# Kernel optimization log

Measured on AMD Instinct MI355X. Metric: run time of the kernel, lower is better.

## Reference

```python
import jax, jax.numpy as jnp
import numpy as np

N = 8192
IN_F = 512
OUT_F = 128
NEG_BIG = -9.0e15


def setup_inputs() -> dict:
    key = jax.random.key(0)
    k_x, k_adj, k_w, k_a1, k_a2 = jax.random.split(key, 5)
    X = jax.random.normal(k_x, (N, IN_F), dtype=jnp.float32)
    adj = jax.random.randint(k_adj, (N, N), 0, 2, dtype=jnp.int32)
    # xavier_uniform with gain=1.414
    gain = 1.414
    lim_w = gain * np.sqrt(6.0 / (IN_F + OUT_F))
    W = jax.random.uniform(k_w, (IN_F, OUT_F), minval=-lim_w, maxval=lim_w, dtype=jnp.float32)
    lim_a = gain * np.sqrt(6.0 / (OUT_F + 1))
    a_1 = jax.random.uniform(k_a1, (OUT_F, 1), minval=-lim_a, maxval=lim_a, dtype=jnp.float32)
    a_2 = jax.random.uniform(k_a2, (OUT_F, 1), minval=-lim_a, maxval=lim_a, dtype=jnp.float32)
    return {"X": X, "adj": adj, "W": W, "a_1": a_1, "a_2": a_2}


def reference(X, adj, W, a_1, a_2):
    h = X @ W                         # [N, out]
    Wh1 = h @ a_1                     # [N, 1]
    Wh2 = h @ a_2                     # [N, 1]
    alpha = Wh1 + Wh2.T               # [N, N] broadcast score sum
    s = jax.nn.sigmoid(alpha)
    masked = jnp.where(adj > 0, s, jnp.float32(NEG_BIG))
    attn = jax.nn.softmax(masked, axis=1)  # dropout p=0.0 -> identity
    return attn @ h                   # [N, out]
```

## Files before the change

### kernel.cpp

```cpp
#include <hip/hip_runtime.h>
#include <hip/hip_bf16.h>

#define N_NODES 8192
#define IN_F 512
#define OUT_F 128
#define KP 16
#define KT_PER 16
#define NWORDS (N_NODES / 32)
#define LOG2E 1.4426950408889634f

typedef unsigned short u16;
typedef unsigned int u32;
typedef short s16x8 __attribute__((ext_vector_type(8)));
typedef float f32x4 __attribute__((ext_vector_type(4)));
typedef u32 u32x4 __attribute__((ext_vector_type(4)));

__device__ __forceinline__ u16 f2bf(float f) {
    union { float f; unsigned u; } x; x.f = f;
    unsigned r = x.u + 0x7FFFu + ((x.u >> 16) & 1u);
    return (u16)(r >> 16);
}

__device__ __forceinline__ u32 packbf2(float a, float b) {
    __hip_bfloat162 h = __float22bfloat162_rn(make_float2(a, b));
    u32 u; __builtin_memcpy(&u, &h, 4);
    return u;
}

__device__ __forceinline__ float edge_p(float wh1, float w2, int keep) {
    float alpha = wh1 + w2;
    float e = exp2f(-LOG2E * alpha);
    float s = __builtin_amdgcn_rcpf(1.0f + e);
    float p = exp2f(LOG2E * s);
    return keep ? p : 0.0f;
}

__global__ __launch_bounds__(256)
void prep(const int* __restrict__ adj, const float* __restrict__ W,
          const float* __restrict__ a1, const float* __restrict__ a2,
          u32* __restrict__ Pk, u16* __restrict__ W_frag,
          float* __restrict__ Wa1, float* __restrict__ Wa2) {
    int b = blockIdx.x;
    int tid = threadIdx.x;
    if (b < 8192) {
        int gid = b * 256 + tid;
        const int* src = adj + (size_t)gid * 32;
        u32 bits = 0;
        #pragma unroll
        for (int t = 0; t < 8; t++) {
            int4 v = *(const int4*)(src + t * 4);
            bits |= (u32)(v.x > 0) << (t * 4 + 0);
            bits |= (u32)(v.y > 0) << (t * 4 + 1);
            bits |= (u32)(v.z > 0) << (t * 4 + 2);
            bits |= (u32)(v.w > 0) << (t * 4 + 3);
        }
        Pk[gid] = bits;
    } else if (b < 8448) {
        int t2 = (b - 8192) * 256 + tid;
        int j = t2 & 7;
        int lane = (t2 >> 3) & 63;
        int nt = (t2 >> 9) & 7;
        int kt = t2 >> 12;
        int k = kt * 32 + (lane >> 4) * 8 + j;
        int n = nt * 16 + (lane & 15);
        W_frag[t2] = f2bf(W[k * OUT_F + n]);
    } else {
        int k = (b - 8448) * 256 + tid;
        float s1 = 0.f, s2 = 0.f;
        #pragma unroll 8
        for (int n = 0; n < OUT_F; n++) {
            float w = W[k * OUT_F + n];
            s1 += w * a1[n];
            s2 += w * a2[n];
        }
        Wa1[k] = s1; Wa2[k] = s2;
    }
}

__global__ __launch_bounds__(512)
void gemm_h(const float* __restrict__ X, const u16* __restrict__ W_frag,
            const float* __restrict__ Wa1, const float* __restrict__ Wa2,
            float* __restrict__ Wh1, float* __restrict__ Wh2,
            u16* __restrict__ h_frag) {
    int tid = threadIdx.x;
    int wave = tid >> 6;
    int lane = tid & 63;
    int quad = lane >> 4;
    int lid = lane & 15;
    int rbase = blockIdx.x * 16;
    const float* xrow = X + (size_t)(rbase + lid) * IN_F;
    const s16x8* Wf = (const s16x8*)W_frag;
    f32x4 acc = {};
    float p1 = 0.f, p2 = 0.f;
    int nt0 = wave;

    int k0p = quad * 8;
    float4 X0 = *(const float4*)(xrow + k0p);
    float4 X1 = *(const float4*)(xrow + k0p + 4);
    s16x8 B0 = Wf[nt0 * 64 + lane];
    float4 A0 = {}, A1 = {}, C0 = {}, C1 = {};
    if (wave == 0) {
        A0 = *(const float4*)(Wa1 + k0p); A1 = *(const float4*)(Wa1 + k0p + 4);
        C0 = *(const float4*)(Wa2 + k0p); C1 = *(const float4*)(Wa2 + k0p + 4);
    }

    #pragma unroll 1
    for (int kt = 0; kt < 16; kt++) {
        float4 x0 = X0, x1 = X1;
        s16x8 b0 = B0;
        float4 wa = A0, wb = A1, wc = C0, wd = C1;
        int ktn = (kt + 1 < 16) ? kt + 1 : kt;
        int k0n = ktn * 32 + quad * 8;
        X0 = *(const float4*)(xrow + k0n);
        X1 = *(const float4*)(xrow + k0n + 4);
        B0 = Wf[(ktn * 8 + nt0) * 64 + lane];
        if (wave == 0) {
            A0 = *(const float4*)(Wa1 + k0n); A1 = *(const float4*)(Wa1 + k0n + 4);
            C0 = *(const float4*)(Wa2 + k0n); C1 = *(const float4*)(Wa2 + k0n + 4);
        }

        u32x4 uv;
        uv.x = packbf2(x0.x, x0.y); uv.y = packbf2(x0.z, x0.w);
        uv.z = packbf2(x1.x, x1.y); uv.w = packbf2(x1.z, x1.w);
        s16x8 a = __builtin_bit_cast(s16x8, uv);
        if (wave == 0) {
            p1 += x0.x*wa.x + x0.y*wa.y + x0.z*wa.z + x0.w*wa.w
                + x1.x*wb.x + x1.y*wb.y + x1.z*wb.z + x1.w*wb.w;
            p2 += x0.x*wc.x + x0.y*wc.y + x0.z*wc.z + x0.w*wc.w
                + x1.x*wd.x + x1.y*wd.y + x1.z*wd.z + x1.w*wd.w;
        }
        acc = __builtin_amdgcn_mfma_f32_16x16x32_bf16(a, b0, acc, 0, 0, 0);
    }

    #pragma unroll
    for (int reg = 0; reg < 4; reg++) {
        int row = rbase + quad * 4 + reg;
        int ktile = row >> 5, kl = row & 31;
        int lane2 = (kl >> 3) * 16 + lid, j2 = kl & 7;
        h_frag[(size_t)((ktile * 8 + nt0) * 64 + lane2) * 8 + j2] = f2bf(acc[reg]);
    }
    if (wave == 0) {
        p1 += __shfl_xor(p1, 16, 64); p1 += __shfl_xor(p1, 32, 64);
        p2 += __shfl_xor(p2, 16, 64); p2 += __shfl_xor(p2, 32, 64);
        if (lane < 16) { Wh1[rbase + lid] = p1; Wh2[rbase + lid] = p2; }
    }
}

__global__ __launch_bounds__(256)
void attn_kernel(const u32* __restrict__ Pk, const float* __restrict__ Wh1,
                 const float* __restrict__ Wh2, const u16* __restrict__ h_frag,
                 float* __restrict__ out_part, float* __restrict__ sum_part) {
    int tid = threadIdx.x;
    int wave = tid >> 6;
    int lane = tid & 63;
    int quad = lane >> 4;
    int lid = lane & 15;
    int rtile = blockIdx.x >> 4;
    int kh = blockIdx.x & (KP - 1);
    int rbase = rtile * 128 + wave * 32;
    int r0 = rbase + lid, r1 = r0 + 16;

    float wh10 = Wh1[r0], wh11 = Wh1[r1];
    f32x4 acc0[8] = {}, acc1[8] = {};
    float ps0 = 0.f, ps1 = 0.f;
    const s16x8* Hf = (const s16x8*)h_frag;
    const u32* prow0 = Pk + (size_t)r0 * NWORDS;
    const u32* prow1 = Pk + (size_t)r1 * NWORDS;
    const int kt0 = kh * KT_PER;

    u32x4 PA = *(const u32x4*)(prow0 + kt0);
    u32x4 PB = *(const u32x4*)(prow1 + kt0);

    auto step = [&](int i, u32 pw0, u32 pw1) {
        int kt = kt0 + i;
        int k0 = kt * 32 + quad * 8;
        float4 w20 = *(const float4*)(Wh2 + k0);
        float4 w21 = *(const float4*)(Wh2 + k0 + 4);
        u32 w0 = pw0 >> (quad * 8);
        u32 w1 = pw1 >> (quad * 8);

        float e0 = edge_p(wh10, w20.x, (w0 >> 0) & 1);
        float e1 = edge_p(wh10, w20.y, (w0 >> 1) & 1);
        float e2 = edge_p(wh10, w20.z, (w0 >> 2) & 1);
        float e3 = edge_p(wh10, w20.w, (w0 >> 3) & 1);
        float e4 = edge_p(wh10, w21.x, (w0 >> 4) & 1);
        float e5 = edge_p(wh10, w21.y, (w0 >> 5) & 1);
        float e6 = edge_p(wh10, w21.z, (w0 >> 6) & 1);
        float e7 = edge_p(wh10, w21.w, (w0 >> 7) & 1);
        ps0 += ((e0 + e1) + (e2 + e3)) + ((e4 + e5) + (e6 + e7));
        u32x4 uv0;
        uv0.x = packbf2(e0, e1); uv0.y = packbf2(e2, e3);
        uv0.z = packbf2(e4, e5); uv0.w = packbf2(e6, e7);

        float f0 = edge_p(wh11, w20.x, (w1 >> 0) & 1);
        float f1 = edge_p(wh11, w20.y, (w1 >> 1) & 1);
        float f2 = edge_p(wh11, w20.z, (w1 >> 2) & 1);
        float f3 = edge_p(wh11, w20.w, (w1 >> 3) & 1);
        float f4 = edge_p(wh11, w21.x, (w1 >> 4) & 1);
        float f5 = edge_p(wh11, w21.y, (w1 >> 5) & 1);
        float f6 = edge_p(wh11, w21.z, (w1 >> 6) & 1);
        float f7 = edge_p(wh11, w21.w, (w1 >> 7) & 1);
        ps1 += ((f0 + f1) + (f2 + f3)) + ((f4 + f5) + (f6 + f7));
        u32x4 uv1;
        uv1.x = packbf2(f0, f1); uv1.y = packbf2(f2, f3);
        uv1.z = packbf2(f4, f5); uv1.w = packbf2(f6, f7);

        s16x8 af0 = __builtin_bit_cast(s16x8, uv0);
        s16x8 af1 = __builtin_bit_cast(s16x8, uv1);

        #pragma unroll
        for (int nt = 0; nt < 8; nt++) {
            s16x8 b = Hf[(kt * 8 + nt) * 64 + lane];
            acc0[nt] = __builtin_amdgcn_mfma_f32_16x16x32_bf16(af0, b, acc0[nt], 0, 0, 0);
            acc1[nt] = __builtin_amdgcn_mfma_f32_16x16x32_bf16(af1, b, acc1[nt], 0, 0, 0);
        }
    };

    #pragma unroll 1
    for (int g = 0; g < KT_PER / 4; g++) {
        u32x4 cPA = PA, cPB = PB;
        int gb = kt0 + ((g + 1 < KT_PER / 4) ? (g + 1) * 4 : 0);
        PA = *(const u32x4*)(prow0 + gb);
        PB = *(const u32x4*)(prow1 + gb);
        step(g * 4 + 0, cPA.x, cPB.x);
        step(g * 4 + 1, cPA.y, cPB.y);
        step(g * 4 + 2, cPA.z, cPB.z);
        step(g * 4 + 3, cPA.w, cPB.w);
    }

    ps0 += __shfl_xor(ps0, 16, 64); ps0 += __shfl_xor(ps0, 32, 64);
    ps1 += __shfl_xor(ps1, 16, 64); ps1 += __shfl_xor(ps1, 32, 64);
    if (quad == 0) {
        sum_part[(size_t)kh * N_NODES + r0] = ps0;
        sum_part[(size_t)kh * N_NODES + r1] = ps1;
    }

    #pragma unroll
    for (int nt = 0; nt < 8; nt++) {
        #pragma unroll
        for (int reg = 0; reg < 4; reg++) {
            int row0 = rbase + quad * 4 + reg;
            int col = nt * 16 + lid;
            out_part[((size_t)kh * N_NODES + row0) * OUT_F + col] = acc0[nt][reg];
            out_part[((size_t)kh * N_NODES + row0 + 16) * OUT_F + col] = acc1[nt][reg];
        }
    }
}

__global__ void finalize(const float* __restrict__ out_part,
                         const float* __restrict__ sum_part,
                         float* __restrict__ out) {
    int gid = blockIdx.x * 256 + threadIdx.x;
    int i = gid >> 7;
    float s = 0.f, v = 0.f;
    for (int kh = 0; kh < KP; kh++) {
        s += sum_part[(size_t)kh * N_NODES + i];
        v += out_part[(size_t)kh * N_NODES * OUT_F + gid];
    }
    out[gid] = v / s;
}

extern "C" void kernel_launch(void* const* d_in, const int* in_sizes, int n_in,
                              void* d_out, int out_size, void* d_ws, size_t ws_size,
                              hipStream_t stream) {
    const float* X   = (const float*)d_in[0];
    const int*   adj = (const int*)d_in[1];
    const float* W   = (const float*)d_in[2];
    const float* a1  = (const float*)d_in[3];
    const float* a2  = (const float*)d_in[4];

    char* ws = (char*)d_ws;
    float* Wh1 = (float*)(ws);
    float* Wh2 = (float*)(ws + (32 << 10));
    float* Wa1 = (float*)(ws + (64 << 10));
    float* Wa2 = (float*)(ws + (66 << 10));
    u16* W_frag = (u16*)(ws + (128 << 10));
    u16* h_frag = (u16*)(ws + (256 << 10));
    u32* Pk     = (u32*)(ws + ((size_t)4 << 20));
    float* out_part = (float*)(ws + ((size_t)16 << 20));
    float* sum_part = (float*)(ws + ((size_t)80 << 20));
    float* out = (float*)d_out;

    hipLaunchKernelGGL(prep, dim3(8450), dim3(256), 0, stream,
                       adj, W, a1, a2, Pk, W_frag, Wa1, Wa2);
    hipLaunchKernelGGL(gemm_h, dim3(512), dim3(512), 0, stream,
                       X, W_frag, Wa1, Wa2, Wh1, Wh2, h_frag);
    hipLaunchKernelGGL(attn_kernel, dim3(64 * KP), dim3(256), 0, stream,
                       Pk, Wh1, Wh2, h_frag, out_part, sum_part);
    hipLaunchKernelGGL(finalize, dim3((N_NODES * OUT_F) / 256), dim3(256), 0, stream,
                       out_part, sum_part, out);
}
```

Baseline: 461.9 us.

## Stage h fragments in LDS, halve K-split, restructure gemm_h with LDS X tiles

The attention kernel now splits K into 8 parts instead of 16. It double-buffers h_frag tiles and Wh2 slices in shared memory, staged cooperatively by all four waves, so they are no longer each loaded per wave from global memory. gemm_h keeps W fragments in registers, stages bf16-packed X tiles through double-buffered LDS, and does 32 rows per block. The Wh1/Wh2 dot products move to separate extra blocks. This cuts redundant global traffic and partial-sum volume, at the cost of less grid parallelism in attention, more LDS and register pressure, and explicit barriers.

```diff
diff --git a/kernel.cpp b/kernel.cpp
--- a/kernel.cpp
+++ b/kernel.cpp
@@ -4,8 +4,8 @@
 #define N_NODES 8192
 #define IN_F 512
 #define OUT_F 128
-#define KP 16
-#define KT_PER 16
+#define KP 8
+#define KT_PER 32
 #define NWORDS (N_NODES / 32)
 #define LOG2E 1.4426950408889634f
 
@@ -77,59 +77,69 @@
     }
 }
 
-__global__ __launch_bounds__(512)
+__global__ __launch_bounds__(512, 2)
 void gemm_h(const float* __restrict__ X, const u16* __restrict__ W_frag,
             const float* __restrict__ Wa1, const float* __restrict__ Wa2,
             float* __restrict__ Wh1, float* __restrict__ Wh2,
             u16* __restrict__ h_frag) {
     int tid = threadIdx.x;
+    if (blockIdx.x >= 256) {
+        int r = (blockIdx.x - 256) * 512 + tid;
+        const float4* xr = (const float4*)(X + (size_t)r * IN_F);
+        const float4* a4 = (const float4*)Wa1;
+        const float4* b4 = (const float4*)Wa2;
+        float s1 = 0.f, s2 = 0.f;
+        #pragma unroll 4
+        for (int i = 0; i < 128; i++) {
+            float4 x = xr[i], a = a4[i], bb = b4[i];
+            s1 += x.x*a.x + x.y*a.y + x.z*a.z + x.w*a.w;
+            s2 += x.x*bb.x + x.y*bb.y + x.z*bb.z + x.w*bb.w;
+        }
+        Wh1[r] = s1; Wh2[r] = s2;
+        return;
+    }
+
+    __shared__ u32x4 AXL[2][512];
     int wave = tid >> 6;
     int lane = tid & 63;
     int quad = lane >> 4;
     int lid = lane & 15;
-    int rbase = blockIdx.x * 16;
-    const float* xrow = X + (size_t)(rbase + lid) * IN_F;
+    int rbase = blockIdx.x * 32;
     const s16x8* Wf = (const s16x8*)W_frag;
-    f32x4 acc = {};
-    float p1 = 0.f, p2 = 0.f;
-    int nt0 = wave;
-
-    int k0p = quad * 8;
-    float4 X0 = *(const float4*)(xrow + k0p);
-    float4 X1 = *(const float4*)(xrow + k0p + 4);
-    s16x8 B0 = Wf[nt0 * 64 + lane];
-    float4 A0 = {}, A1 = {}, C0 = {}, C1 = {};
-    if (wave == 0) {
-        A0 = *(const float4*)(Wa1 + k0p); A1 = *(const float4*)(Wa1 + k0p + 4);
-        C0 = *(const float4*)(Wa2 + k0p); C1 = *(const float4*)(Wa2 + k0p + 4);
-    }
-
-    #pragma unroll 1
-    for (int kt = 0; kt < 16; kt++) {
-        float4 x0 = X0, x1 = X1;
-        s16x8 b0 = B0;
-        float4 wa = A0, wb = A1, wc = C0, wd = C1;
-        int ktn = (kt + 1 < 16) ? kt + 1 : kt;
-        int k0n = ktn * 32 + quad * 8;
-        X0 = *(const float4*)(xrow + k0n);
-        X1 = *(const float4*)(xrow + k0n + 4);
-        B0 = Wf[(ktn * 8 + nt0) * 64 + lane];
-        if (wave == 0) {
-            A0 = *(const float4*)(Wa1 + k0n); A1 = *(const float4*)(Wa1 + k0n + 4);
-            C0 = *(const float4*)(Wa2 + k0n); C1 = *(const float4*)(Wa2 + k0n + 4);
-        }
-
-        u32x4 uv;
-        uv.x = packbf2(x0.x, x0.y); uv.y = packbf2(x0.z, x0.w);
-        uv.z = packbf2(x1.x, x1.y); uv.w = packbf2(x1.z, x1.w);
-        s16x8 a = __builtin_bit_cast(s16x8, uv);
-        if (wave == 0) {
-            p1 += x0.x*wa.x + x0.y*wa.y + x0.z*wa.z + x0.w*wa.w
-                + x1.x*wb.x + x1.y*wb.y + x1.z*wb.z + x1.w*wb.w;
-            p2 += x0.x*wc.x + x0.y*wc.y + x0.z*wc.z + x0.w*wc.w
-                + x1.x*wd.x + x1.y*wd.y + x1.z*wd.z + x1.w*wd.w;
-        }
-        acc = __builtin_amdgcn_mfma_f32_16x16x32_bf16(a, b0, acc, 0, 0, 0);
+
+    s16x8 Wr[16];
+    #pragma unroll
+    for (int kt = 0; kt < 16; kt++) Wr[kt] = Wf[(kt * 8 + wave) * 64 + lane];
+
+    int s_tile = tid >> 8, s_ktl = (tid >> 6) & 3, s_lane = tid & 63;
+    int s_row = rbase + s_tile * 16 + (s_lane & 15);
+    const float* s_base = X + (size_t)s_row * IN_F + (s_lane >> 4) * 8;
+
+    f32x4 acc0 = {}, acc1 = {};
+    float4 x0 = *(const float4*)(s_base + s_ktl * 32);
+    float4 x1 = *(const float4*)(s_base + s_ktl * 32 + 4);
+
+    #pragma unroll
+    for (int c = 0; c < 4; c++) {
+        asm volatile("s_waitcnt vmcnt(0)" ::: "memory");
+        u32x4 v;
+        v.x = packbf2(x0.x, x0.y); v.y = packbf2(x0.z, x0.w);
+        v.z = packbf2(x1.x, x1.y); v.w = packbf2(x1.z, x1.w);
+        AXL[c & 1][tid] = v;
+        int cn = (c + 1 < 4) ? c + 1 : c;
+        x0 = *(const float4*)(s_base + (cn * 4 + s_ktl) * 32);
+        x1 = *(const float4*)(s_base + (cn * 4 + s_ktl) * 32 + 4);
+        asm volatile("s_waitcnt lgkmcnt(0)" ::: "memory");
+        __builtin_amdgcn_s_barrier();
+        __builtin_amdgcn_sched_barrier(0);
+        const s16x8* AB = (const s16x8*)&AXL[c & 1][0];
+        #pragma unroll
+        for (int ktl = 0; ktl < 4; ktl++) {
+            s16x8 a0 = AB[ktl * 64 + lane];
+            s16x8 a1 = AB[256 + ktl * 64 + lane];
+            acc0 = __builtin_amdgcn_mfma_f32_16x16x32_bf16(a0, Wr[c * 4 + ktl], acc0, 0, 0, 0);
+            acc1 = __builtin_amdgcn_mfma_f32_16x16x32_bf16(a1, Wr[c * 4 + ktl], acc1, 0, 0, 0);
+        }
     }
 
     #pragma unroll
@@ -137,25 +147,27 @@
         int row = rbase + quad * 4 + reg;
         int ktile = row >> 5, kl = row & 31;
         int lane2 = (kl >> 3) * 16 + lid, j2 = kl & 7;
-        h_frag[(size_t)((ktile * 8 + nt0) * 64 + lane2) * 8 + j2] = f2bf(acc[reg]);
-    }
-    if (wave == 0) {
-        p1 += __shfl_xor(p1, 16, 64); p1 += __shfl_xor(p1, 32, 64);
-        p2 += __shfl_xor(p2, 16, 64); p2 += __shfl_xor(p2, 32, 64);
-        if (lane < 16) { Wh1[rbase + lid] = p1; Wh2[rbase + lid] = p2; }
-    }
-}
-
-__global__ __launch_bounds__(256)
+        h_frag[(size_t)((ktile * 8 + wave) * 64 + lane2) * 8 + j2] = f2bf(acc0[reg]);
+        int row1 = row + 16;
+        int ktile1 = row1 >> 5, kl1 = row1 & 31;
+        int lane21 = (kl1 >> 3) * 16 + lid, j21 = kl1 & 7;
+        h_frag[(size_t)((ktile1 * 8 + wave) * 64 + lane21) * 8 + j21] = f2bf(acc1[reg]);
+    }
+}
+
+__global__ __launch_bounds__(256, 2)
 void attn_kernel(const u32* __restrict__ Pk, const float* __restrict__ Wh1,
                  const float* __restrict__ Wh2, const u16* __restrict__ h_frag,
                  float* __restrict__ out_part, float* __restrict__ sum_part) {
+    __shared__ u32x4 HfL[2][2048];
+    __shared__ float Wh2L[1024];
+
     int tid = threadIdx.x;
     int wave = tid >> 6;
     int lane = tid & 63;
     int quad = lane >> 4;
     int lid = lane & 15;
-    int rtile = blockIdx.x >> 4;
+    int rtile = blockIdx.x >> 3;
     int kh = blockIdx.x & (KP - 1);
     int rbase = rtile * 128 + wave * 32;
     int r0 = rbase + lid, r1 = r0 + 16;
@@ -163,19 +175,21 @@
     float wh10 = Wh1[r0], wh11 = Wh1[r1];
     f32x4 acc0[8] = {}, acc1[8] = {};
     float ps0 = 0.f, ps1 = 0.f;
-    const s16x8* Hf = (const s16x8*)h_frag;
-    const u32* prow0 = Pk + (size_t)r0 * NWORDS;
-    const u32* prow1 = Pk + (size_t)r1 * NWORDS;
-    const int kt0 = kh * KT_PER;
-
-    u32x4 PA = *(const u32x4*)(prow0 + kt0);
-    u32x4 PB = *(const u32x4*)(prow1 + kt0);
-
-    auto step = [&](int i, u32 pw0, u32 pw1) {
-        int kt = kt0 + i;
-        int k0 = kt * 32 + quad * 8;
-        float4 w20 = *(const float4*)(Wh2 + k0);
-        float4 w21 = *(const float4*)(Wh2 + k0 + 4);
+    const u32x4* Hg = (const u32x4*)h_frag + (size_t)(kh * KT_PER) * 512;
+    const u32* prow0 = Pk + (size_t)r0 * NWORDS + kh * KT_PER;
+    const u32* prow1 = Pk + (size_t)r1 * NWORDS + kh * KT_PER;
+
+    ((float4*)Wh2L)[tid] = ((const float4*)Wh2)[kh * 256 + tid];
+    u32x4 st[8];
+    #pragma unroll
+    for (int i = 0; i < 8; i++) st[i] = Hg[i * 256 + tid];
+    u32x4 P0r = *(const u32x4*)(prow0);
+    u32x4 P1r = *(const u32x4*)(prow1);
+
+    auto step = [&](int ktg, u32 pw0, u32 pw1, const s16x8* HB) {
+        int ktl = ktg & 3;
+        float4 w20 = *(const float4*)&Wh2L[ktg * 32 + quad * 8];
+        float4 w21 = *(const float4*)&Wh2L[ktg * 32 + quad * 8 + 4];
         u32 w0 = pw0 >> (quad * 8);
         u32 w1 = pw1 >> (quad * 8);
 
@@ -210,22 +224,33 @@
 
         #pragma unroll
         for (int nt = 0; nt < 8; nt++) {
-            s16x8 b = Hf[(kt * 8 + nt) * 64 + lane];
+            s16x8 b = HB[(ktl * 8 + nt) * 64 + lane];
             acc0[nt] = __builtin_amdgcn_mfma_f32_16x16x32_bf16(af0, b, acc0[nt], 0, 0, 0);
             acc1[nt] = __builtin_amdgcn_mfma_f32_16x16x32_bf16(af1, b, acc1[nt], 0, 0, 0);
         }
     };
 
     #pragma unroll 1
-    for (int g = 0; g < KT_PER / 4; g++) {
-        u32x4 cPA = PA, cPB = PB;
-        int gb = kt0 + ((g + 1 < KT_PER / 4) ? (g + 1) * 4 : 0);
-        PA = *(const u32x4*)(prow0 + gb);
-        PB = *(const u32x4*)(prow1 + gb);
-        step(g * 4 + 0, cPA.x, cPB.x);
-        step(g * 4 + 1, cPA.y, cPB.y);
-        step(g * 4 + 2, cPA.z, cPB.z);
-        step(g * 4 + 3, cPA.w, cPB.w);
+    for (int c = 0; c < 8; c++) {
+        asm volatile("s_waitcnt vmcnt(0)" ::: "memory");
+        u32x4* dst = &HfL[c & 1][0];
+        #pragma unroll
+        for (int i = 0; i < 8; i++) dst[i * 256 + tid] = st[i];
+        u32x4 cP0 = P0r, cP1 = P1r;
+        int cn = (c + 1 < 8) ? c + 1 : c;
+        const u32x4* src = Hg + cn * 2048;
+        #pragma unroll
+        for (int i = 0; i < 8; i++) st[i] = src[i * 256 + tid];
+        P0r = *(const u32x4*)(prow0 + cn * 4);
+        P1r = *(const u32x4*)(prow1 + cn * 4);
+        asm volatile("s_waitcnt lgkmcnt(0)" ::: "memory");
+        __builtin_amdgcn_s_barrier();
+        __builtin_amdgcn_sched_barrier(0);
+        const s16x8* HB = (const s16x8*)&HfL[c & 1][0];
+        step(c * 4 + 0, cP0.x, cP1.x, HB);
+        step(c * 4 + 1, cP0.y, cP1.y, HB);
+        step(c * 4 + 2, cP0.z, cP1.z, HB);
+        step(c * 4 + 3, cP0.w, cP1.w, HB);
     }
 
     ps0 += __shfl_xor(ps0, 16, 64); ps0 += __shfl_xor(ps0, 32, 64);
@@ -278,12 +303,12 @@
     u16* h_frag = (u16*)(ws + (256 << 10));
     u32* Pk     = (u32*)(ws + ((size_t)4 << 20));
     float* out_part = (float*)(ws + ((size_t)16 << 20));
-    float* sum_part = (float*)(ws + ((size_t)80 << 20));
+    float* sum_part = (float*)(ws + ((size_t)48 << 20));
     float* out = (float*)d_out;
 
     hipLaunchKernelGGL(prep, dim3(8450), dim3(256), 0, stream,
                        adj, W, a1, a2, Pk, W_frag, Wa1, Wa2);
-    hipLaunchKernelGGL(gemm_h, dim3(512), dim3(512), 0, stream,
+    hipLaunchKernelGGL(gemm_h, dim3(272), dim3(512), 0, stream,
                        X, W_frag, Wa1, Wa2, Wh1, Wh2, h_frag);
     hipLaunchKernelGGL(attn_kernel, dim3(64 * KP), dim3(256), 0, stream,
                        Pk, Wh1, Wh2, h_frag, out_part, sum_part);
```

Result: slower. 510.1 us (+10.4%).
